# Kernel tuning notes

Hardware: AMD Instinct MI355X
Metric: run time of the kernel (lower is better)

## Reference

```python
import jax, jax.numpy as jnp
import numpy as np

B, T, I, H, K, C, TH, CLS = 128, 512, 300, 150, 6, 300, 20, 5

def setup_inputs() -> dict:
    key = jax.random.key(0)
    ks = jax.random.split(key, 16)
    s = lambda *sh: 1.0 / np.sqrt(sh[-1])
    inp = {
        "x": jax.random.normal(ks[0], (B, T, I), jnp.float32),
        # GRU params (PyTorch layout: [3H, in]) for fwd/bwd directions
        "Wih_f": jax.random.normal(ks[1], (3 * H, I), jnp.float32) * s(3 * H, I),
        "Whh_f": jax.random.normal(ks[2], (3 * H, H), jnp.float32) * s(3 * H, H),
        "bih_f": jax.random.normal(ks[3], (3 * H,), jnp.float32) * 0.01,
        "bhh_f": jax.random.normal(ks[4], (3 * H,), jnp.float32) * 0.01,
        "Wih_b": jax.random.normal(ks[5], (3 * H, I), jnp.float32) * s(3 * H, I),
        "Whh_b": jax.random.normal(ks[6], (3 * H, H), jnp.float32) * s(3 * H, H),
        "bih_b": jax.random.normal(ks[7], (3 * H,), jnp.float32) * 0.01,
        "bhh_b": jax.random.normal(ks[8], (3 * H,), jnp.float32) * 0.01,
        # topic attention params (stacked over K topics)
        "attn_context": jax.random.normal(ks[9], (K, C), jnp.float32),
        "Wattn": jax.random.normal(ks[10], (K, C + 2 * H, 2 * H), jnp.float32) * s(1, C + 2 * H),
        "battn": jax.random.normal(ks[11], (K, 2 * H), jnp.float32) * 0.01,
        "Wtop": jax.random.normal(ks[12], (K, 2 * H, TH), jnp.float32) * s(1, 2 * H),
        "btop": jax.random.normal(ks[13], (K, TH), jnp.float32) * 0.01,
        "Wout": jax.random.normal(ks[14], (K * TH, CLS), jnp.float32) * s(1, K * TH),
        "bout": jax.random.normal(ks[15], (CLS,), jnp.float32) * 0.01,
    }
    return inp

def _gru_dir(x, Wih, Whh, bih, bhh, reverse):
    # x: [B,T,I] -> outputs [B,T,H], final hidden [B,H]
    xT = jnp.swapaxes(x, 0, 1)                    # [T,B,I]
    if reverse:
        xT = xT[::-1]
    gi = xT @ Wih.T + bih                         # [T,B,3H] input projections (one big GEMM)
    h0 = jnp.zeros((x.shape[0], Whh.shape[1]), x.dtype)
    def step(h, g):
        gh = h @ Whh.T + bhh
        i_r, i_z, i_n = jnp.split(g, 3, axis=-1)
        h_r, h_z, h_n = jnp.split(gh, 3, axis=-1)
        r = jax.nn.sigmoid(i_r + h_r)
        z = jax.nn.sigmoid(i_z + h_z)
        n = jnp.tanh(i_n + r * h_n)
        h_new = (1.0 - z) * n + z * h
        return h_new, h_new
    hT, ys = jax.lax.scan(step, h0, gi)
    if reverse:
        ys = ys[::-1]
    return jnp.swapaxes(ys, 0, 1), hT

def reference(x, Wih_f, Whh_f, bih_f, bhh_f, Wih_b, Whh_b, bih_b, bhh_b,
              attn_context, Wattn, battn, Wtop, btop, Wout, bout):
    # eval mode: dropout is identity
    out_f, h_f = _gru_dir(x, Wih_f, Whh_f, bih_f, bhh_f, False)
    out_b, h_b = _gru_dir(x, Wih_b, Whh_b, bih_b, bhh_b, True)
    seq = jnp.concatenate([out_f, out_b], axis=-1)       # [B,T,2H]
    hidden = jnp.concatenate([h_f, h_b], axis=-1)        # [B,2H]
    Bsz = x.shape[0]
    Kt = attn_context.shape[0]
    # per-topic context: cat(context_k, hidden) -> linear -> tanh, batched over topics
    ctx_in = jnp.concatenate([
        jnp.broadcast_to(attn_context[None, :, :], (Bsz, Kt, attn_context.shape[1])),
        jnp.broadcast_to(hidden[:, None, :], (Bsz, Kt, hidden.shape[1])),
    ], axis=-1)                                          # [B,K,C+2H]
    context = jnp.tanh(jnp.einsum('bkc,kcd->bkd', ctx_in, Wattn) + battn)  # [B,K,2H]
    # attention pooling over time, all topics at once
    energy = jnp.einsum('btd,bkd->btk', seq, context)    # [B,T,K]
    probs = jax.nn.softmax(energy, axis=1)
    pooled = jnp.einsum('btd,btk->bkd', seq, probs)      # [B,K,2H]
    topic = jax.nn.relu(jnp.einsum('bkd,kdh->bkh', pooled, Wtop) + btop)   # [B,K,TH]
    feats = topic.reshape(Bsz, -1)                       # [B,K*TH]
    logits = feats @ Wout + bout
    out = jax.nn.softmax(logits, axis=1)                 # eval + validate=False path
    # regularization loss on normalized contexts
    nc = context / jnp.linalg.norm(context, axis=2, keepdims=True).clip(1e-12)
    G = jnp.einsum('bkd,bjd->bkj', nc, nc)               # [B,K,K]
    diff = G - jnp.eye(Kt, dtype=G.dtype)[None]
    reg = jnp.mean(jnp.sqrt(jnp.sum(diff * diff, axis=(1, 2))))
    return out, reg
```

## Files before the change

### kernel.cpp

```cpp
#include <hip/hip_runtime.h>
#include <hip/hip_bf16.h>
#include <math.h>

#define Bq   128
#define Tq   512
#define Iq   300
#define Hq   150
#define G3   450
#define Kq   6
#define Cq   300
#define D2   300
#define THq  20
#define CLSq 5

typedef __attribute__((ext_vector_type(8))) short short8;
typedef __attribute__((ext_vector_type(4))) float floatx4;

__global__ __launch_bounds__(256) void cast_bf16_kernel(
    const float* __restrict__ in, __hip_bfloat16* __restrict__ out, int n4)
{
    const int i = blockIdx.x * 256 + threadIdx.x;
    if (i < n4) {
        float4 v = *(const float4*)(in + 4 * (size_t)i);
        out[4 * (size_t)i + 0] = __float2bfloat16(v.x);
        out[4 * (size_t)i + 1] = __float2bfloat16(v.y);
        out[4 * (size_t)i + 2] = __float2bfloat16(v.z);
        out[4 * (size_t)i + 3] = __float2bfloat16(v.w);
    }
}

#define LB 40

__global__ __launch_bounds__(256) void gi_gemm_mfma(
    const __hip_bfloat16* __restrict__ xb,
    const __hip_bfloat16* __restrict__ Wbf,
    const float* __restrict__ bf_, const float* __restrict__ bb_,
    float* __restrict__ gic, int t0f, int t0b, int tcShift)
{
    const int dir = blockIdx.z;
    const unsigned short* W = (const unsigned short*)(Wbf + (size_t)dir * G3 * Iq);
    const unsigned short* X = (const unsigned short*)xb;
    const float* bias = dir ? bb_ : bf_;
    const int t0 = dir ? t0b : t0f;
    const int TCr = 1 << tcShift;
    float* outb = gic + (size_t)dir * Bq * TCr * G3;

    const int m0 = blockIdx.y * 128;
    const int n0 = blockIdx.x * 128;
    const int tid  = threadIdx.x;
    const int wv   = tid >> 6, lane = tid & 63;
    const int wm   = wv & 1,  wn   = wv >> 1;
    const int quad = lane >> 4, mr = lane & 15;

    __shared__ __align__(16) unsigned short Ab[128 * LB];
    __shared__ __align__(16) unsigned short Bb[128 * LB];

    floatx4 acc[4][4];
    #pragma unroll
    for (int i = 0; i < 4; ++i)
        #pragma unroll
        for (int j = 0; j < 4; ++j)
            acc[i][j] = (floatx4){0.f, 0.f, 0.f, 0.f};

    for (int k0 = 0; k0 < 320; k0 += 32) {
        __syncthreads();
        #pragma unroll
        for (int i = 0; i < 4; ++i) {
            const int g = tid + 256 * i;
            const int row = g >> 3, kq = g & 7;
            const int k = k0 + kq * 4;
            const int r = m0 + row;
            const int bb2 = r >> tcShift, lt = r & (TCr - 1);
            ushort4 av = make_ushort4(0, 0, 0, 0);
            if (k < Iq)
                av = *(const ushort4*)(X + ((size_t)bb2 * Tq + t0 + lt) * Iq + k);
            *(ushort4*)&Ab[row * LB + kq * 4] = av;
            const int n = n0 + row;
            ushort4 bv = make_ushort4(0, 0, 0, 0);
            if (n < G3 && k < Iq)
                bv = *(const ushort4*)(W + (size_t)n * Iq + k);
            *(ushort4*)&Bb[row * LB + kq * 4] = bv;
        }
        __syncthreads();

        short8 af[4], bfr[4];
        #pragma unroll
        for (int i = 0; i < 4; ++i)
            af[i] = *(const short8*)&Ab[(wm * 64 + i * 16 + mr) * LB + quad * 8];
        #pragma unroll
        for (int j = 0; j < 4; ++j)
            bfr[j] = *(const short8*)&Bb[(wn * 64 + j * 16 + mr) * LB + quad * 8];
        #pragma unroll
        for (int i = 0; i < 4; ++i)
            #pragma unroll
            for (int j = 0; j < 4; ++j)
                acc[i][j] = __builtin_amdgcn_mfma_f32_16x16x32_bf16(
                    af[i], bfr[j], acc[i][j], 0, 0, 0);
    }

    #pragma unroll
    for (int j = 0; j < 4; ++j) {
        const int gn = n0 + wn * 64 + j * 16 + mr;
        if (gn >= G3) continue;
        const float bv = bias[gn];
        #pragma unroll
        for (int i = 0; i < 4; ++i) {
            const int mbase = m0 + wm * 64 + i * 16 + quad * 4;
            #pragma unroll
            for (int rg = 0; rg < 4; ++rg)
                outb[(size_t)(mbase + rg) * G3 + gn] = acc[i][j][rg] + bv;
        }
    }
}

__global__ __launch_bounds__(512, 2) void gru_rec(
    const float* __restrict__ gic,
    const float* __restrict__ Whh_f, const float* __restrict__ bhh_f,
    const float* __restrict__ Whh_b, const float* __restrict__ bhh_b,
    float* __restrict__ hstate,
    float* __restrict__ seq,
    int chunk, int tcShift)
{
    const int TCr = 1 << tcShift;
    const int bid = blockIdx.x;
    const int dir = bid & 1;
    const int b   = bid >> 1;
    const float* Whh = dir ? Whh_b : Whh_f;
    const float* bhh = dir ? bhh_b : bhh_f;
    const int tid = threadIdx.x;
    const bool gemv = (tid < G3);
    const bool gate = (tid >= 300 && tid < G3);
    const int t = tid - 300;

    __shared__ __align__(16) float stage[64 * 150];
    __shared__ __align__(16) float hbuf[152];
    __shared__ float sArr[300];

    float w[152];
    w[150] = 0.f; w[151] = 0.f;
    if (gemv) {
        const float* wr = Whh + (size_t)tid * Hq;
        #pragma unroll
        for (int q = 0; q < 75; ++q) {
            const float2 v = *(const float2*)(wr + 2 * q);
            w[2 * q]     = v.x;
            w[2 * q + 1] = v.y;
        }
    } else {
        #pragma unroll
        for (int c = 0; c < 150; ++c) w[c] = 0.f;
    }
    const float bh = gemv ? bhh[tid] : 0.f;

    float* hs = hstate + (size_t)(dir * Bq + b) * Hq;
    float hprev = 0.f;
    if (gate && chunk > 0) hprev = hs[t];

    if (tid < 152)
        hbuf[tid] = (tid < Hq && chunk > 0) ? hs[tid] : 0.f;
    __syncthreads();

    const float* gib = gic + (size_t)(dir * Bq + b) * TCr * G3;
    const int t0 = dir ? (Tq - TCr * (chunk + 1)) : (chunk * TCr);
    float* seqb = seq + (size_t)b * Tq * D2 + dir * Hq;
    const float4* hb4 = (const float4*)hbuf;

    const int lt0 = dir ? (TCr - 1) : 0;
    float gval = gemv ? gib[(size_t)lt0 * G3 + tid] : 0.f;

    for (int s = 0; s < TCr; ++s) {
        const int ltn = dir ? (TCr - 2 - s) : (s + 1);
        float gnext = 0.f;
        if (s + 1 < TCr && gemv)
            gnext = gib[(size_t)ltn * G3 + tid];

        float ghn = 0.f;
        if (gemv) {
            float acc = bh + ((tid < 300) ? gval : 0.f);
            #pragma unroll
            for (int q = 0; q < 38; ++q) {
                const float4 hv = hb4[q];
                acc += hv.x * w[4*q]   + hv.y * w[4*q+1]
                     + hv.z * w[4*q+2] + hv.w * w[4*q+3];
            }
            if (tid < 300) sArr[tid] = acc;
            else           ghn = acc;
        }
        __syncthreads();

        if (gate) {
            const float r  = 1.f / (1.f + __expf(-sArr[t]));
            const float z  = 1.f / (1.f + __expf(-sArr[150 + t]));
            const float nv = tanhf(gval + r * ghn);
            const float hn = (1.f - z) * nv + z * hprev;
            hprev = hn;
            hbuf[t] = hn;
            stage[(s & 63) * 150 + t] = hn;
        }
        __syncthreads();

        if ((s & 63) == 63 || s == TCr - 1) {
            const int sf0 = s & ~63;
            const int nf2 = (s - sf0 + 1) * 75;
            for (int idx = tid; idx < nf2; idx += 512) {
                const int rrow = idx / 75, cc = idx % 75;
                const int ss = sf0 + rrow;
                const int ltw = dir ? (TCr - 1 - ss) : ss;
                *(float2*)(seqb + (size_t)(t0 + ltw) * D2 + 2 * cc) =
                    *(const float2*)&stage[rrow * 150 + 2 * cc];
            }
        }

        gval = gnext;
    }

    if (gate) hs[t] = hprev;
}

__global__ void ctxw_kernel(
    const float* __restrict__ attn_context,
    const float* __restrict__ Wattn,
    const float* __restrict__ battn,
    float* __restrict__ ctxW)
{
    const int o = blockIdx.x * 256 + threadIdx.x;
    if (o >= Kq * D2) return;
    const int k = o / D2, d = o % D2;
    float acc = battn[o];
    const float* Wp = Wattn + ((size_t)k * (Cq + D2)) * D2 + d;
    for (int c = 0; c < Cq; ++c)
        acc += attn_context[k * Cq + c] * Wp[(size_t)c * D2];
    ctxW[o] = acc;
}

__global__ __launch_bounds__(256) void ctx_compute(
    const float* __restrict__ seq,
    const float* __restrict__ Wattn,
    const float* __restrict__ ctxW,
    float* __restrict__ context,
    float* __restrict__ normsq)
{
    const int b = blockIdx.x;
    const int k = blockIdx.y;
    const int tid = threadIdx.x;
    const int lane = tid & 63, wv = tid >> 6;

    __shared__ float hb[304];
    __shared__ float red[4];

    for (int i = tid; i < D2; i += 256)
        hb[i] = (i < Hq) ? seq[((size_t)b * Tq + (Tq - 1)) * D2 + i]
                         : seq[(size_t)b * Tq * D2 + i];
    __syncthreads();

    float ssq = 0.f;
    for (int d = tid; d < D2; d += 256) {
        float acc = ctxW[k * D2 + d];
        const float* Wp = Wattn + ((size_t)k * (Cq + D2) + Cq) * D2 + d;
        for (int jj = 0; jj < D2; ++jj)
            acc += hb[jj] * Wp[(size_t)jj * D2];
        const float c = tanhf(acc);
        context[((size_t)b * Kq + k) * D2 + d] = c;
        ssq += c * c;
    }
    for (int off = 32; off > 0; off >>= 1) ssq += __shfl_xor(ssq, off, 64);
    if (lane == 0) red[wv] = ssq;
    __syncthreads();
    if (tid == 0) normsq[b * Kq + k] = red[0] + red[1] + red[2] + red[3];
}

__global__ __launch_bounds__(256) void gram_kernel(
    const float* __restrict__ context,
    const float* __restrict__ normsq,
    float* __restrict__ regbuf)
{
    const int b = blockIdx.x;
    const int tid = threadIdx.x;
    __shared__ float ctx[Kq * D2];
    __shared__ float Gm[36];

    for (int o = tid; o < Kq * D2; o += 256)
        ctx[o] = context[(size_t)b * Kq * D2 + o];
    __syncthreads();

    if (tid < 36) {
        const int k = tid / 6, jj = tid % 6;
        float g = 0.f;
        for (int d = 0; d < D2; ++d)
            g += ctx[k * D2 + d] * ctx[jj * D2 + d];
        const float nk = fmaxf(sqrtf(normsq[b * Kq + k]), 1e-12f);
        const float nj = fmaxf(sqrtf(normsq[b * Kq + jj]), 1e-12f);
        g /= (nk * nj);
        const float diff = g - ((k == jj) ? 1.f : 0.f);
        Gm[tid] = diff * diff;
    }
    __syncthreads();
    if (tid == 0) {
        float s = 0.f;
        for (int i = 0; i < 36; ++i) s += Gm[i];
        regbuf[b] = sqrtf(s);
    }
}

__global__ __launch_bounds__(256) void energy_kernel(
    const float* __restrict__ seq,
    const float* __restrict__ context,
    float* __restrict__ en)
{
    const int tc = blockIdx.x;
    const int b  = blockIdx.y;
    const int tid = threadIdx.x;
    const int lane = tid & 63, wv = tid >> 6;

    __shared__ float ctx[Kq * D2];
    for (int o = tid; o < Kq * D2; o += 256)
        ctx[o] = context[(size_t)b * Kq * D2 + o];
    __syncthreads();

    const float* seqb = seq + (size_t)b * Tq * D2;
    for (int s = 0; s < 16; ++s) {
        const int tt = tc * 64 + s * 4 + wv;
        float acc[Kq] = {0.f,0.f,0.f,0.f,0.f,0.f};
        for (int d = lane; d < D2; d += 64) {
            const float sv = seqb[(size_t)tt * D2 + d];
            #pragma unroll
            for (int k = 0; k < Kq; ++k) acc[k] += sv * ctx[k * D2 + d];
        }
        #pragma unroll
        for (int k = 0; k < Kq; ++k) {
            float v = acc[k];
            for (int off = 32; off > 0; off >>= 1) v += __shfl_xor(v, off, 64);
            if (lane == 0) en[((size_t)b * Tq + tt) * Kq + k] = v;
        }
    }
}

__global__ __launch_bounds__(256) void softmax_kernel(float* __restrict__ en)
{
    const int b = blockIdx.x;
    const int tid = threadIdx.x;
    const int lane = tid & 63, wv = tid >> 6;
    __shared__ float es[Tq * Kq];
    __shared__ float red[8];

    for (int o = tid; o < Tq * Kq; o += 256)
        es[o] = en[(size_t)b * Tq * Kq + o];
    __syncthreads();

    for (int k = 0; k < Kq; ++k) {
        float m = -1e30f;
        for (int tt = tid; tt < Tq; tt += 256) m = fmaxf(m, es[tt * Kq + k]);
        for (int off = 32; off > 0; off >>= 1) m = fmaxf(m, __shfl_xor(m, off, 64));
        if (lane == 0) red[wv] = m;
        __syncthreads();
        m = fmaxf(fmaxf(red[0], red[1]), fmaxf(red[2], red[3]));
        float ssum = 0.f;
        for (int tt = tid; tt < Tq; tt += 256) {
            const float e = __expf(es[tt * Kq + k] - m);
            es[tt * Kq + k] = e;
            ssum += e;
        }
        for (int off = 32; off > 0; off >>= 1) ssum += __shfl_xor(ssum, off, 64);
        if (lane == 0) red[4 + wv] = ssum;
        __syncthreads();
        const float inv = 1.f / (red[4] + red[5] + red[6] + red[7]);
        for (int tt = tid; tt < Tq; tt += 256) es[tt * Kq + k] *= inv;
        __syncthreads();
    }

    for (int o = tid; o < Tq * Kq; o += 256)
        en[(size_t)b * Tq * Kq + o] = es[o];
}

__global__ __launch_bounds__(256) void pooledp_kernel(
    const float* __restrict__ seq,
    const float* __restrict__ en,
    float* __restrict__ partial)
{
    const int tc = blockIdx.x;
    const int b  = blockIdx.y;
    const int tid = threadIdx.x;
    const int lane = tid & 63, wv = tid >> 6;

    __shared__ float pr[64 * Kq];
    __shared__ float part[4][Kq * D2];

    if (tid < 64 * Kq / 2) {
        pr[tid]       = en[((size_t)b * Tq + tc * 64) * Kq + tid];
        pr[tid + 192] = en[((size_t)b * Tq + tc * 64) * Kq + tid + 192];
    }
    __syncthreads();

    const float* seqb = seq + (size_t)b * Tq * D2;

    float pp[Kq][5];
    #pragma unroll
    for (int k = 0; k < Kq; ++k)
        #pragma unroll
        for (int q = 0; q < 5; ++q) pp[k][q] = 0.f;

    for (int s = 0; s < 16; ++s) {
        const int tl = s * 4 + wv;
        const int tt = tc * 64 + tl;
        float prr[Kq];
        #pragma unroll
        for (int k = 0; k < Kq; ++k) prr[k] = pr[tl * Kq + k];
        #pragma unroll
        for (int q = 0; q < 5; ++q) {
            const int d = lane + q * 64;
            const float sv = (d < D2) ? seqb[(size_t)tt * D2 + d] : 0.f;
            #pragma unroll
            for (int k = 0; k < Kq; ++k) pp[k][q] += prr[k] * sv;
        }
    }
    #pragma unroll
    for (int k = 0; k < Kq; ++k)
        #pragma unroll
        for (int q = 0; q < 5; ++q) {
            const int d = lane + q * 64;
            if (d < D2) part[wv][k * D2 + d] = pp[k][q];
        }
    __syncthreads();
    float* op = partial + ((size_t)b * 8 + tc) * (Kq * D2);
    for (int o = tid; o < Kq * D2; o += 256)
        op[o] = part[0][o] + part[1][o] + part[2][o] + part[3][o];
}

__global__ __launch_bounds__(256) void final_kernel(
    const float* __restrict__ partial,
    const float* __restrict__ Wtop,
    const float* __restrict__ btop,
    const float* __restrict__ Wout,
    const float* __restrict__ bout,
    float* __restrict__ outp)
{
    const int b = blockIdx.x;
    const int tid = threadIdx.x;
    __shared__ float pooled[Kq * D2];
    __shared__ float feats[Kq * THq];
    __shared__ float lsm[8];

    for (int o = tid; o < Kq * D2; o += 256) {
        float s = 0.f;
        #pragma unroll
        for (int c = 0; c < 8; ++c)
            s += partial[((size_t)b * 8 + c) * (Kq * D2) + o];
        pooled[o] = s;
    }
    __syncthreads();

    if (tid < Kq * THq) {
        const int k = tid / THq, hh = tid % THq;
        float acc = btop[tid];
        const float* wp = Wtop + (size_t)k * D2 * THq + hh;
        for (int d = 0; d < D2; ++d)
            acc += pooled[k * D2 + d] * wp[(size_t)d * THq];
        feats[tid] = fmaxf(acc, 0.f);
    }
    __syncthreads();

    if (tid < CLSq) {
        float acc = bout[tid];
        for (int f = 0; f < Kq * THq; ++f)
            acc += feats[f] * Wout[f * CLSq + tid];
        lsm[tid] = acc;
    }
    __syncthreads();
    if (tid < CLSq) {
        float m = lsm[0];
        for (int c = 1; c < CLSq; ++c) m = fmaxf(m, lsm[c]);
        float s = 0.f;
        for (int c = 0; c < CLSq; ++c) s += __expf(lsm[c] - m);
        outp[(size_t)b * CLSq + tid] = __expf(lsm[tid] - m) / s;
    }
}

__global__ void reg_final(const float* __restrict__ regbuf, float* __restrict__ outp)
{
    const int tid = threadIdx.x;
    float v = regbuf[tid];
    for (int off = 32; off > 0; off >>= 1) v += __shfl_xor(v, off, 64);
    __shared__ float r2[2];
    if ((tid & 63) == 0) r2[tid >> 6] = v;
    __syncthreads();
    if (tid == 0) outp[Bq * CLSq] = (r2[0] + r2[1]) * (1.f / (float)Bq);
}

extern "C" void kernel_launch(void* const* d_in, const int* in_sizes, int n_in,
                              void* d_out, int out_size, void* d_ws, size_t ws_size,
                              hipStream_t stream)
{
    const float* x     = (const float*)d_in[0];
    const float* Wih_f = (const float*)d_in[1];
    const float* Whh_f = (const float*)d_in[2];
    const float* bih_f = (const float*)d_in[3];
    const float* bhh_f = (const float*)d_in[4];
    const float* Wih_b = (const float*)d_in[5];
    const float* Whh_b = (const float*)d_in[6];
    const float* bih_b = (const float*)d_in[7];
    const float* bhh_b = (const float*)d_in[8];
    const float* attn_context = (const float*)d_in[9];
    const float* Wattn = (const float*)d_in[10];
    const float* battn = (const float*)d_in[11];
    const float* Wtop  = (const float*)d_in[12];
    const float* btop  = (const float*)d_in[13];
    const float* Wout  = (const float*)d_in[14];
    const float* bout  = (const float*)d_in[15];
    float* outp = (float*)d_out;

    float* ws       = (float*)d_ws;
    float* seqv     = ws;
    float* hstate   = seqv + (size_t)Bq * Tq * D2;
    float* ctxW     = hstate + (size_t)2 * Bq * Hq;
    float* context  = ctxW + Kq * D2;
    float* regbuf   = context + (size_t)Bq * Kq * D2;
    float* normsq   = regbuf + Bq;
    float* en       = normsq + Bq * Kq;
    float* partial  = en + (size_t)Bq * Tq * Kq;
    __hip_bfloat16* xb16 = (__hip_bfloat16*)(partial + (size_t)Bq * 8 * Kq * D2);
    __hip_bfloat16* Wb16 = xb16 + (size_t)Bq * Tq * Iq;
    float* gi_chunk = (float*)(Wb16 + (size_t)2 * G3 * Iq);
    const size_t fixed_floats = (size_t)(gi_chunk - ws);

    int tcShift = 5;
    for (int sh = 8; sh >= 5; --sh) {
        size_t need = (fixed_floats + (size_t)115200 * (1 << sh)) * 4;
        if (need <= ws_size) { tcShift = sh; break; }
    }
    const int TCr = 1 << tcShift;
    const int NL = Tq / TCr;

    cast_bf16_kernel<<<dim3((Bq * Tq * Iq / 4 + 255) / 256), 256, 0, stream>>>(
        x, xb16, Bq * Tq * Iq / 4);
    cast_bf16_kernel<<<dim3((G3 * Iq / 4 + 255) / 256), 256, 0, stream>>>(
        Wih_f, Wb16, G3 * Iq / 4);
    cast_bf16_kernel<<<dim3((G3 * Iq / 4 + 255) / 256), 256, 0, stream>>>(
        Wih_b, Wb16 + (size_t)G3 * Iq, G3 * Iq / 4);

    for (int c = 0; c < NL; ++c) {
        const int t0f = c * TCr;
        const int t0b = Tq - TCr * (c + 1);
        gi_gemm_mfma<<<dim3(4, Bq * TCr / 128, 2), 256, 0, stream>>>(
            xb16, Wb16, bih_f, bih_b, gi_chunk, t0f, t0b, tcShift);
        gru_rec<<<dim3(2 * Bq), 512, 0, stream>>>(
            gi_chunk, Whh_f, bhh_f, Whh_b, bhh_b, hstate, seqv, c, tcShift);
    }

    ctxw_kernel<<<dim3((Kq * D2 + 255) / 256), 256, 0, stream>>>(
        attn_context, Wattn, battn, ctxW);
    ctx_compute<<<dim3(Bq, Kq), 256, 0, stream>>>(seqv, Wattn, ctxW, context, normsq);
    gram_kernel<<<dim3(Bq), 256, 0, stream>>>(context, normsq, regbuf);
    energy_kernel<<<dim3(8, Bq), 256, 0, stream>>>(seqv, context, en);
    softmax_kernel<<<dim3(Bq), 256, 0, stream>>>(en);
    pooledp_kernel<<<dim3(8, Bq), 256, 0, stream>>>(seqv, en, partial);
    final_kernel<<<dim3(Bq), 256, 0, stream>>>(partial, Wtop, btop, Wout, bout, outp);
    reg_final<<<dim3(1), 128, 0, stream>>>(regbuf, outp);
}
```

Baseline: 1.254 ms.

## Store GRU recurrent weights as fp16 in LDS and use packed dot2

Recurrent weights Whh are pre-cast to fp16, padded to 152 columns, and loaded into shared memory per block instead of being held as 150 fp32 registers per thread. The hidden state is kept as packed fp16 and the matvec uses v_dot2 fp16 instructions with four independent accumulators. The staged, batched write of the output sequence is replaced by direct per-step global stores, which also removes one sync path. This aims to cut register pressure and per-step ALU work, at the cost of fp16 rounding in the recurrence and ~137KB of LDS per block, which limits blocks per CU.

```diff
diff --git a/kernel.cpp b/kernel.cpp
--- a/kernel.cpp
+++ b/kernel.cpp
@@ -15,6 +15,7 @@
 
 typedef __attribute__((ext_vector_type(8))) short short8;
 typedef __attribute__((ext_vector_type(4))) float floatx4;
+typedef _Float16 h2v __attribute__((ext_vector_type(2)));
 
 __global__ __launch_bounds__(256) void cast_bf16_kernel(
     const float* __restrict__ in, __hip_bfloat16* __restrict__ out, int n4)
@@ -27,6 +28,21 @@
         out[4 * (size_t)i + 2] = __float2bfloat16(v.z);
         out[4 * (size_t)i + 3] = __float2bfloat16(v.w);
     }
+}
+
+__global__ __launch_bounds__(256) void cast_whh_f16(
+    const float* __restrict__ Wf, const float* __restrict__ Wb,
+    unsigned short* __restrict__ out)
+{
+    const int idx = blockIdx.x * 256 + threadIdx.x;
+    const int total = 2 * G3 * 152;
+    if (idx >= total) return;
+    const int dir = idx / (G3 * 152);
+    const int rem = idx % (G3 * 152);
+    const int r = rem / 152, c = rem % 152;
+    float v = 0.f;
+    if (c < Hq) v = (dir ? Wb : Wf)[(size_t)r * Hq + c];
+    out[idx] = __builtin_bit_cast(unsigned short, (_Float16)v);
 }
 
 #define LB 40
@@ -113,10 +129,22 @@
     }
 }
 
-__global__ __launch_bounds__(512, 2) void gru_rec(
+__device__ __forceinline__ float dot2h(unsigned int w, unsigned int h, float c)
+{
+#if __has_builtin(__builtin_amdgcn_fdot2)
+    return __builtin_amdgcn_fdot2(__builtin_bit_cast(h2v, w),
+                                  __builtin_bit_cast(h2v, h), c, false);
+#else
+    const h2v a = __builtin_bit_cast(h2v, w);
+    const h2v b = __builtin_bit_cast(h2v, h);
+    return c + (float)a.x * (float)b.x + (float)a.y * (float)b.y;
+#endif
+}
+
+__global__ __launch_bounds__(512) void gru_rec(
     const float* __restrict__ gic,
-    const float* __restrict__ Whh_f, const float* __restrict__ bhh_f,
-    const float* __restrict__ Whh_b, const float* __restrict__ bhh_b,
+    const unsigned short* __restrict__ W16,
+    const float* __restrict__ bhh_f, const float* __restrict__ bhh_b,
     float* __restrict__ hstate,
     float* __restrict__ seq,
     int chunk, int tcShift)
@@ -125,65 +153,72 @@
     const int bid = blockIdx.x;
     const int dir = bid & 1;
     const int b   = bid >> 1;
-    const float* Whh = dir ? Whh_b : Whh_f;
     const float* bhh = dir ? bhh_b : bhh_f;
     const int tid = threadIdx.x;
-    const bool gemv = (tid < G3);
-    const bool gate = (tid >= 300 && tid < G3);
-    const int t = tid - 300;
-
-    __shared__ __align__(16) float stage[64 * 150];
-    __shared__ __align__(16) float hbuf[152];
+    const int row = tid;
+    const bool gemv = (row < G3);
+    const bool gate = (row >= 300 && row < G3);
+    const int t = row - 300;
+
+    __shared__ __align__(16) unsigned int Wlds[G3 * 76];
+    __shared__ __align__(16) unsigned int h2b[80];
     __shared__ float sArr[300];
 
-    float w[152];
-    w[150] = 0.f; w[151] = 0.f;
-    if (gemv) {
-        const float* wr = Whh + (size_t)tid * Hq;
-        #pragma unroll
-        for (int q = 0; q < 75; ++q) {
-            const float2 v = *(const float2*)(wr + 2 * q);
-            w[2 * q]     = v.x;
-            w[2 * q + 1] = v.y;
-        }
-    } else {
-        #pragma unroll
-        for (int c = 0; c < 150; ++c) w[c] = 0.f;
-    }
-    const float bh = gemv ? bhh[tid] : 0.f;
+    {
+        const uint4* Wg = (const uint4*)(W16 + (size_t)dir * G3 * 152);
+        uint4* Wl = (uint4*)Wlds;
+        for (int i = tid; i < G3 * 19; i += 512) Wl[i] = Wg[i];
+    }
+
+    const float bh = gemv ? bhh[row] : 0.f;
 
     float* hs = hstate + (size_t)(dir * Bq + b) * Hq;
     float hprev = 0.f;
     if (gate && chunk > 0) hprev = hs[t];
 
-    if (tid < 152)
-        hbuf[tid] = (tid < Hq && chunk > 0) ? hs[tid] : 0.f;
+    if (tid < 80) {
+        unsigned int v = 0;
+        if (tid < 76 && chunk > 0) {
+            const float lo = (2 * tid     < Hq) ? hs[2 * tid]     : 0.f;
+            const float hi = (2 * tid + 1 < Hq) ? hs[2 * tid + 1] : 0.f;
+            h2v p; p.x = (_Float16)lo; p.y = (_Float16)hi;
+            v = __builtin_bit_cast(unsigned int, p);
+        }
+        h2b[tid] = v;
+    }
     __syncthreads();
 
     const float* gib = gic + (size_t)(dir * Bq + b) * TCr * G3;
     const int t0 = dir ? (Tq - TCr * (chunk + 1)) : (chunk * TCr);
     float* seqb = seq + (size_t)b * Tq * D2 + dir * Hq;
-    const float4* hb4 = (const float4*)hbuf;
-
-    const int lt0 = dir ? (TCr - 1) : 0;
-    float gval = gemv ? gib[(size_t)lt0 * G3 + tid] : 0.f;
+
+    const uint4* wr4 = (const uint4*)(Wlds + row * 76);
+    const uint4* h4  = (const uint4*)h2b;
+
+    int lt = dir ? (TCr - 1) : 0;
+    float gval = gemv ? gib[(size_t)lt * G3 + row] : 0.f;
 
     for (int s = 0; s < TCr; ++s) {
         const int ltn = dir ? (TCr - 2 - s) : (s + 1);
         float gnext = 0.f;
         if (s + 1 < TCr && gemv)
-            gnext = gib[(size_t)ltn * G3 + tid];
+            gnext = gib[(size_t)ltn * G3 + row];
 
         float ghn = 0.f;
         if (gemv) {
-            float acc = bh + ((tid < 300) ? gval : 0.f);
+            float a0 = bh + ((row < 300) ? gval : 0.f);
+            float a1 = 0.f, a2 = 0.f, a3 = 0.f;
             #pragma unroll
-            for (int q = 0; q < 38; ++q) {
-                const float4 hv = hb4[q];
-                acc += hv.x * w[4*q]   + hv.y * w[4*q+1]
-                     + hv.z * w[4*q+2] + hv.w * w[4*q+3];
+            for (int j = 0; j < 19; ++j) {
+                const uint4 w = wr4[j];
+                const uint4 h = h4[j];
+                a0 = dot2h(w.x, h.x, a0);
+                a1 = dot2h(w.y, h.y, a1);
+                a2 = dot2h(w.z, h.z, a2);
+                a3 = dot2h(w.w, h.w, a3);
             }
-            if (tid < 300) sArr[tid] = acc;
+            const float acc = (a0 + a1) + (a2 + a3);
+            if (row < 300) sArr[row] = acc;
             else           ghn = acc;
         }
         __syncthreads();
@@ -194,24 +229,13 @@
             const float nv = tanhf(gval + r * ghn);
             const float hn = (1.f - z) * nv + z * hprev;
             hprev = hn;
-            hbuf[t] = hn;
-            stage[(s & 63) * 150 + t] = hn;
-        }
-        __syncthreads();
-
-        if ((s & 63) == 63 || s == TCr - 1) {
-            const int sf0 = s & ~63;
-            const int nf2 = (s - sf0 + 1) * 75;
-            for (int idx = tid; idx < nf2; idx += 512) {
-                const int rrow = idx / 75, cc = idx % 75;
-                const int ss = sf0 + rrow;
-                const int ltw = dir ? (TCr - 1 - ss) : ss;
-                *(float2*)(seqb + (size_t)(t0 + ltw) * D2 + 2 * cc) =
-                    *(const float2*)&stage[rrow * 150 + 2 * cc];
-            }
-        }
+            ((_Float16*)h2b)[t] = (_Float16)hn;
+            seqb[(size_t)(t0 + lt) * D2 + t] = hn;
+        }
+        __syncthreads();
 
         gval = gnext;
+        lt = ltn;
     }
 
     if (gate) hs[t] = hprev;
@@ -519,7 +543,8 @@
     float* partial  = en + (size_t)Bq * Tq * Kq;
     __hip_bfloat16* xb16 = (__hip_bfloat16*)(partial + (size_t)Bq * 8 * Kq * D2);
     __hip_bfloat16* Wb16 = xb16 + (size_t)Bq * Tq * Iq;
-    float* gi_chunk = (float*)(Wb16 + (size_t)2 * G3 * Iq);
+    unsigned short* W16 = (unsigned short*)(Wb16 + (size_t)2 * G3 * Iq);
+    float* gi_chunk = (float*)(W16 + (size_t)2 * G3 * 152);
     const size_t fixed_floats = (size_t)(gi_chunk - ws);
 
     int tcShift = 5;
@@ -536,6 +561,8 @@
         Wih_f, Wb16, G3 * Iq / 4);
     cast_bf16_kernel<<<dim3((G3 * Iq / 4 + 255) / 256), 256, 0, stream>>>(
         Wih_b, Wb16 + (size_t)G3 * Iq, G3 * Iq / 4);
+    cast_whh_f16<<<dim3((2 * G3 * 152 + 255) / 256), 256, 0, stream>>>(
+        Whh_f, Whh_b, W16);
 
     for (int c = 0; c < NL; ++c) {
         const int t0f = c * TCr;
@@ -543,7 +570,7 @@
         gi_gemm_mfma<<<dim3(4, Bq * TCr / 128, 2), 256, 0, stream>>>(
             xb16, Wb16, bih_f, bih_b, gi_chunk, t0f, t0b, tcShift);
         gru_rec<<<dim3(2 * Bq), 512, 0, stream>>>(
-            gi_chunk, Whh_f, bhh_f, Whh_b, bhh_b, hstate, seqv, c, tcShift);
+            gi_chunk, W16, bhh_f, bhh_b, hstate, seqv, c, tcShift);
     }
 
     ctxw_kernel<<<dim3((Kq * D2 + 255) / 256), 256, 0, stream>>>(
```

New measurement: 1.114 ms. 1.13x faster.
